# Performance work log

Hardware: AMD Instinct MI355X
Metric: run time of the kernel (lower is better)

The kernel has to match this reference:

```python
import jax, jax.numpy as jnp
import numpy as np

EMBED_DIM = 1024
NUM_HEADS = 16
HEAD_DIM = EMBED_DIM // NUM_HEADS

def setup_inputs() -> dict:
    key = jax.random.key(0)
    k1, k2, k3 = jax.random.split(key, 3)
    x = jax.random.normal(k1, (4, 2048, EMBED_DIM), dtype=jnp.float32)
    # Linear weights stored as [out, in] like torch; we apply x @ W.T
    W_qkv = jax.random.normal(k2, (3 * EMBED_DIM, EMBED_DIM), dtype=jnp.float32) * (EMBED_DIM ** -0.5)
    W_proj = jax.random.normal(k3, (EMBED_DIM, EMBED_DIM), dtype=jnp.float32) * (EMBED_DIM ** -0.5)
    return {"x": x, "W_qkv": W_qkv, "W_proj": W_proj}

def reference(x, W_qkv, W_proj):
    B, T, C = x.shape
    H, D = NUM_HEADS, HEAD_DIM
    qkv = x @ W_qkv.T                          # [B,T,3C]
    q, k, v = jnp.split(qkv, 3, axis=-1)
    q = q.reshape(B, T, H, D).transpose(0, 2, 1, 3)  # [B,H,T,D]
    k = k.reshape(B, T, H, D).transpose(0, 2, 1, 3)
    v = v.reshape(B, T, H, D).transpose(0, 2, 1, 3)
    scores = jnp.einsum('bhqd,bhkd->bhqk', q, k) / jnp.sqrt(jnp.asarray(D, x.dtype))
    causal = jnp.tril(jnp.ones((T, T), dtype=bool))
    scores = jnp.where(causal, scores, -jnp.inf)
    weights = jax.nn.softmax(scores, axis=-1)
    out = jnp.einsum('bhqk,bhkd->bhqd', weights, v)  # [B,H,T,D]
    out = out.transpose(0, 2, 1, 3).reshape(B, T, C)
    return out @ W_proj.T
```

## Files before the change

kernel.cpp:

```cpp
#include <hip/hip_runtime.h>

#define T_SEQ 2048
#define NB 4
#define NH 16
#define HD 64
#define CDIM 1024
#define MROWS (NB * T_SEQ)

typedef __attribute__((ext_vector_type(8))) short short8;
typedef __attribute__((ext_vector_type(4))) float floatx4;

static __device__ __forceinline__ unsigned short f2bf(float f) {
  union { float f; unsigned int i; } c; c.f = f;
  return (unsigned short)((c.i + 0x7FFFu + ((c.i >> 16) & 1u)) >> 16);
}
static __device__ __forceinline__ unsigned short f2bf_trunc(float f) {
  union { float f; unsigned int i; } c; c.f = f;
  return (unsigned short)(c.i >> 16);
}

static __device__ __forceinline__ void gl2lds16(const void* g, void* l) {
  __builtin_amdgcn_global_load_lds(
      (const __attribute__((address_space(1))) unsigned int*)g,
      (__attribute__((address_space(3))) unsigned int*)l, 16, 0, 0);
}

#define X4 (MROWS * CDIM / 4)
#define WQ4 (3 * CDIM * CDIM / 4)
#define WP4 (CDIM * CDIM / 4)
__global__ __launch_bounds__(256) void cast3_bf16(const float* __restrict__ x,
                                                  const float* __restrict__ wq,
                                                  const float* __restrict__ wp,
                                                  unsigned short* __restrict__ out) {
  const int i = blockIdx.x * 256 + threadIdx.x;
  const float* src; int off;
  if (i < X4) { src = x; off = i; }
  else if (i < X4 + WQ4) { src = wq; off = i - X4; }
  else { src = wp; off = i - X4 - WQ4; }
  const float4 v = ((const float4*)src)[off];
  ushort4 o;
  o.x = f2bf(v.x); o.y = f2bf(v.y); o.z = f2bf(v.z); o.w = f2bf(v.w);
  ((ushort4*)out)[i] = o;
}

#define Q_PRESCALE 0.18033688f

#define QNT (CDIM / 64)

__global__ __launch_bounds__(512, 2) void gemm_bf16_qkv256(
    const unsigned short* __restrict__ A,
    const unsigned short* __restrict__ B,
    unsigned short* __restrict__ Oq,
    unsigned short* __restrict__ Ok,
    unsigned short* __restrict__ Ovt,
    const int K)
{
  __shared__ __align__(16) unsigned short As[2][2][128 * 64];
  __shared__ __align__(16) unsigned short Bs[2][2][128 * 64];
  const int tid = threadIdx.x;
  const int w = tid >> 6, l = tid & 63;
  const int quad = l >> 4, l15 = l & 15;
  const int wr = w >> 2, wc = w & 3;
  const int m0 = blockIdx.y * 256, n0 = blockIdx.x * 256;

  const int lrow = l >> 3;
  const int lch = ((l & 7) ^ lrow) * 8;
  const unsigned short* Ag = A + (size_t)(m0 + w * 16 + lrow) * K + lch;
  const unsigned short* Bg = B + (size_t)(n0 + w * 16 + lrow) * K + lch;
  const int ld0 = w * 1024, ld1 = w * 1024 + 512;
  const size_t rsk = (size_t)8 * K;

#define STAGE_A(buf, h, kof) do { \
    gl2lds16(Ag + (size_t)(h) * 128 * K + (kof), &As[buf][h][ld0]); \
    gl2lds16(Ag + (size_t)(h) * 128 * K + rsk + (kof), &As[buf][h][ld1]); } while (0)
#define STAGE_B(buf, h, kof) do { \
    gl2lds16(Bg + (size_t)(h) * 128 * K + (kof), &Bs[buf][h][ld0]); \
    gl2lds16(Bg + (size_t)(h) * 128 * K + rsk + (kof), &Bs[buf][h][ld1]); } while (0)

  const int sw7 = l15 & 7;
  const int co0 = (quad ^ sw7) * 8;
  const int co1 = co0 ^ 32;
  const int fb = l15 * 64;
  const unsigned short* Aw0 = &As[0][wr][0];
  const unsigned short* Aw1 = &As[1][wr][0];
  const unsigned short* Bw0 = &Bs[0][wc >> 1][(wc & 1) * 4096];
  const unsigned short* Bw1 = &Bs[1][wc >> 1][(wc & 1) * 4096];

  floatx4 acc[8][4];
#pragma unroll
  for (int mi = 0; mi < 8; ++mi)
#pragma unroll
    for (int ni = 0; ni < 4; ++ni) acc[mi][ni] = (floatx4){0.f, 0.f, 0.f, 0.f};

  STAGE_A(0, 0, 0); STAGE_A(0, 1, 0); STAGE_B(0, 0, 0); STAGE_B(0, 1, 0);
  STAGE_B(1, 0, 64); STAGE_A(1, 0, 64);
  asm volatile("s_waitcnt vmcnt(4)" ::: "memory");
  __builtin_amdgcn_s_barrier();

#pragma unroll 1
  for (int j = 0; j < QNT; ++j) {
    const int cur = j & 1, nxt = cur ^ 1;
    const unsigned short* Ac = cur ? Aw1 : Aw0;
    const unsigned short* Bc = cur ? Bw1 : Bw0;
    const int kA = (j + 1) * 64, kC = (j + 2) * 64;
    short8 aF[2][4], bL[2][2], bH[2][2];

#pragma unroll
    for (int mi = 0; mi < 4; ++mi) {
      aF[0][mi] = *(const short8*)(Ac + mi * 1024 + fb + co0);
      aF[1][mi] = *(const short8*)(Ac + mi * 1024 + fb + co1);
    }
#pragma unroll
    for (int ni = 0; ni < 2; ++ni) {
      bL[0][ni] = *(const short8*)(Bc + ni * 1024 + fb + co0);
      bL[1][ni] = *(const short8*)(Bc + ni * 1024 + fb + co1);
    }
    if (j + 1 < QNT) STAGE_A(nxt, 1, kA);
    __builtin_amdgcn_s_barrier();
    asm volatile("s_waitcnt lgkmcnt(0)" ::: "memory");
    __builtin_amdgcn_s_setprio(1);
#pragma unroll
    for (int ks = 0; ks < 2; ++ks)
#pragma unroll
      for (int mi = 0; mi < 4; ++mi)
#pragma unroll
        for (int ni = 0; ni < 2; ++ni)
          acc[mi][ni] = __builtin_amdgcn_mfma_f32_16x16x32_bf16(
              bL[ks][ni], aF[ks][mi], acc[mi][ni], 0, 0, 0);
    __builtin_amdgcn_s_setprio(0);
    __builtin_amdgcn_s_barrier();

#pragma unroll
    for (int ni = 0; ni < 2; ++ni) {
      bH[0][ni] = *(const short8*)(Bc + (ni + 2) * 1024 + fb + co0);
      bH[1][ni] = *(const short8*)(Bc + (ni + 2) * 1024 + fb + co1);
    }
    if (j + 1 < QNT) STAGE_B(nxt, 1, kA);
    __builtin_amdgcn_s_barrier();
    asm volatile("s_waitcnt lgkmcnt(0)" ::: "memory");
    __builtin_amdgcn_s_setprio(1);
#pragma unroll
    for (int ks = 0; ks < 2; ++ks)
#pragma unroll
      for (int mi = 0; mi < 4; ++mi)
#pragma unroll
        for (int ni = 0; ni < 2; ++ni)
          acc[mi][ni + 2] = __builtin_amdgcn_mfma_f32_16x16x32_bf16(
              bH[ks][ni], aF[ks][mi], acc[mi][ni + 2], 0, 0, 0);
    __builtin_amdgcn_s_setprio(0);
    __builtin_amdgcn_s_barrier();

#pragma unroll
    for (int mi = 0; mi < 4; ++mi) {
      aF[0][mi] = *(const short8*)(Ac + (mi + 4) * 1024 + fb + co0);
      aF[1][mi] = *(const short8*)(Ac + (mi + 4) * 1024 + fb + co1);
    }
    if (j + 2 < QNT) STAGE_B(cur, 0, kC);
    __builtin_amdgcn_s_barrier();
    asm volatile("s_waitcnt lgkmcnt(0)" ::: "memory");
    __builtin_amdgcn_s_setprio(1);
#pragma unroll
    for (int ks = 0; ks < 2; ++ks)
#pragma unroll
      for (int mi = 0; mi < 4; ++mi)
#pragma unroll
        for (int ni = 0; ni < 2; ++ni)
          acc[mi + 4][ni] = __builtin_amdgcn_mfma_f32_16x16x32_bf16(
              bL[ks][ni], aF[ks][mi], acc[mi + 4][ni], 0, 0, 0);
    __builtin_amdgcn_s_setprio(0);
    __builtin_amdgcn_s_barrier();

    if (j + 2 < QNT) {
      STAGE_A(cur, 0, kC);
      asm volatile("s_waitcnt vmcnt(4)" ::: "memory");
    } else {
      asm volatile("s_waitcnt vmcnt(0)" ::: "memory");
    }
    __builtin_amdgcn_s_barrier();
    __builtin_amdgcn_s_setprio(1);
#pragma unroll
    for (int ks = 0; ks < 2; ++ks)
#pragma unroll
      for (int mi = 0; mi < 4; ++mi)
#pragma unroll
        for (int ni = 0; ni < 2; ++ni)
          acc[mi + 4][ni + 2] = __builtin_amdgcn_mfma_f32_16x16x32_bf16(
              bH[ks][ni], aF[ks][mi], acc[mi + 4][ni + 2], 0, 0, 0);
    __builtin_amdgcn_s_setprio(0);
    __builtin_amdgcn_s_barrier();
  }
#undef STAGE_A
#undef STAGE_B

  const int which = n0 >> 10;
  if (which < 2) {
    unsigned short* dst = (which == 0) ? Oq : Ok;
    const float sc = (which == 0) ? Q_PRESCALE : 1.0f;
#pragma unroll
    for (int ni = 0; ni < 4; ++ni) {
      const int n = n0 + wc * 64 + ni * 16 + quad * 4;
      const int h = (n >> 6) & (NH - 1), d = n & (HD - 1);
#pragma unroll
      for (int mi = 0; mi < 8; ++mi) {
        const int m = m0 + wr * 128 + mi * 16 + l15;
        const int b = m >> 11, t = m & (T_SEQ - 1);
        ushort4 pk;
        pk.x = f2bf(acc[mi][ni][0] * sc); pk.y = f2bf(acc[mi][ni][1] * sc);
        pk.z = f2bf(acc[mi][ni][2] * sc); pk.w = f2bf(acc[mi][ni][3] * sc);
        *(ushort4*)(dst + (((size_t)(b * NH + h) * T_SEQ + t) << 6) + d) = pk;
      }
    }
  } else {
#pragma unroll
    for (int ni = 0; ni < 4; ++ni) {
      const int nb = n0 + wc * 64 + ni * 16 + quad * 4;
      const int h = (nb >> 6) & (NH - 1);
#pragma unroll
      for (int mi = 0; mi < 8; ++mi) {
        const int m = m0 + wr * 128 + mi * 16 + l15;
        const int b = m >> 11, t = m & (T_SEQ - 1);
#pragma unroll
        for (int r = 0; r < 4; ++r) {
          const int d = (nb + r) & (HD - 1);
          Ovt[((size_t)((b * NH + h) * HD + d) << 11) + t] = f2bf(acc[mi][ni][r]);
        }
      }
    }
  }
}

__global__ __launch_bounds__(256) void gemm_bf16_proj(
    const unsigned short* __restrict__ A,
    const unsigned short* __restrict__ B,
    float* __restrict__ O,
    const int N, const int K)
{
  __shared__ unsigned short As[2][128 * 32];
  __shared__ unsigned short Bs[2][128 * 32];
  const int tid = threadIdx.x;
  const int w = tid >> 6, l = tid & 63;
  const int quad = l >> 4, l15 = l & 15;
  const int m0 = blockIdx.y * 128, n0 = blockIdx.x * 128;
  const int wm = (w >> 1) * 64, wn = (w & 1) * 64;
  const int srow = l >> 2;
  const int scol = ((l & 3) ^ (srow & 3)) * 8;

  floatx4 acc[4][4];
#pragma unroll
  for (int mi = 0; mi < 4; ++mi)
#pragma unroll
    for (int ni = 0; ni < 4; ++ni) acc[mi][ni] = (floatx4){0.f, 0.f, 0.f, 0.f};

  const unsigned short* Ag = A + (size_t)(m0 + w * 32 + srow) * K + scol;
  const unsigned short* Bg = B + (size_t)(n0 + w * 32 + srow) * K + scol;
  const int d0 = (w * 32) * 32, d1 = (w * 32 + 16) * 32;
  const int sq = quad ^ (l15 & 3);

  gl2lds16(Ag, &As[0][d0]);
  gl2lds16(Ag + (size_t)16 * K, &As[0][d1]);
  gl2lds16(Bg, &Bs[0][d0]);
  gl2lds16(Bg + (size_t)16 * K, &Bs[0][d1]);

  for (int k0 = 0; k0 < K; k0 += 32) {
    const int cur = (k0 >> 5) & 1, nxt = 1 - cur;
    __syncthreads();
    if (k0 + 32 < K) {
      gl2lds16(Ag + k0 + 32, &As[nxt][d0]);
      gl2lds16(Ag + (size_t)16 * K + k0 + 32, &As[nxt][d1]);
      gl2lds16(Bg + k0 + 32, &Bs[nxt][d0]);
      gl2lds16(Bg + (size_t)16 * K + k0 + 32, &Bs[nxt][d1]);
    }
    short8 af[4], bfr[4];
#pragma unroll
    for (int mi = 0; mi < 4; ++mi)
      af[mi] = *(const short8*)&As[cur][(wm + mi * 16 + l15) * 32 + sq * 8];
#pragma unroll
    for (int ni = 0; ni < 4; ++ni)
      bfr[ni] = *(const short8*)&Bs[cur][(wn + ni * 16 + l15) * 32 + sq * 8];
#pragma unroll
    for (int mi = 0; mi < 4; ++mi)
#pragma unroll
      for (int ni = 0; ni < 4; ++ni)
        acc[mi][ni] = __builtin_amdgcn_mfma_f32_16x16x32_bf16(bfr[ni], af[mi], acc[mi][ni], 0, 0, 0);
  }

#pragma unroll
  for (int ni = 0; ni < 4; ++ni) {
    const int n = n0 + wn + ni * 16 + quad * 4;
#pragma unroll
    for (int mi = 0; mi < 4; ++mi) {
      const int m = m0 + wm + mi * 16 + l15;
      *(float4*)(O + (size_t)m * N + n) =
          make_float4(acc[mi][ni][0], acc[mi][ni][1], acc[mi][ni][2], acc[mi][ni][3]);
    }
  }
}

#define TK 64
#define PTP 72

__global__ __launch_bounds__(512) void attn_mfma(
    const unsigned short* __restrict__ Q,
    const unsigned short* __restrict__ K,
    const unsigned short* __restrict__ Vt,
    unsigned short* __restrict__ O)
{
  __shared__ unsigned short Ks[2][TK * HD];
  __shared__ unsigned short Vts[2][HD * TK];
  __shared__ unsigned short Pt[8][16 * PTP];
  const int tid = threadIdx.x;
  const int w = tid >> 6, l = tid & 63;
  const int quad = l >> 4, l15 = l & 15;
  const int drow = 8 * w + (l >> 3);
  const int dch = ((l & 7) ^ (l >> 3)) * 8;
  const int sw7 = l15 & 7;

  const int bh = blockIdx.x & 63;
  const int pp = blockIdx.x >> 6;
  const int b = bh >> 4, h = bh & 15;
  const size_t hoff = (size_t)bh * T_SEQ * HD;
  const unsigned short* Qh = Q + hoff;
  const unsigned short* Kdma = K + hoff + (size_t)drow * HD + dch;
  const unsigned short* Vdma = Vt + hoff + ((size_t)drow << 11) + dch;
  const int wb = w * 512;

  short8 ones;
#pragma unroll
  for (int j = 0; j < 8; ++j) ones[j] = (short)0x3F80;

#pragma unroll 1
  for (int ii = 0; ii < 2; ++ii) {
    const int qtile = ii ? pp : (15 - pp);
    const int qw = qtile * 128 + w * 16;

    short8 qf[2];
    {
      const int qrow = qw + l15;
      qf[0] = *(const short8*)(Qh + (size_t)qrow * HD + quad * 8);
      qf[1] = *(const short8*)(Qh + (size_t)qrow * HD + 32 + quad * 8);
    }

    floatx4 Of[4];
#pragma unroll
    for (int dc = 0; dc < 4; ++dc) Of[dc] = (floatx4){0.f, 0.f, 0.f, 0.f};
    floatx4 lacc = (floatx4){0.f, 0.f, 0.f, 0.f};

    const int nkt = 2 * qtile + 2;
    __syncthreads();
    gl2lds16(Kdma, &Ks[0][wb]);
    gl2lds16(Vdma, &Vts[0][wb]);

    for (int kt = 0; kt < nkt; ++kt) {
      const int kt0 = kt * TK;
      const int cur = kt & 1, nxt = 1 - cur;
      __syncthreads();
      if (kt + 1 < nkt) {
        gl2lds16(Kdma + (size_t)(kt0 + TK) * HD, &Ks[nxt][wb]);
        gl2lds16(Vdma + kt0 + TK, &Vts[nxt][wb]);
      }

      if (qw + 15 >= kt0) {
        floatx4 Sf[4];
#pragma unroll
        for (int cb = 0; cb < 4; ++cb) {
          Sf[cb] = (floatx4){0.f, 0.f, 0.f, 0.f};
          const int krow = cb * 16 + l15;
#pragma unroll
          for (int h2 = 0; h2 < 2; ++h2) {
            const int ch = (h2 * 4 + quad) ^ sw7;
            const short8 kf = *(const short8*)&Ks[cur][krow * 64 + ch * 8];
            Sf[cb] = __builtin_amdgcn_mfma_f32_16x16x32_bf16(kf, qf[h2], Sf[cb], 0, 0, 0);
          }
        }
        const bool full = (kt0 + 63 <= qw);
        const int q = qw + l15;
#pragma unroll
        for (int cb = 0; cb < 4; ++cb) {
          const int key0 = kt0 + cb * 16 + quad * 4;
          ushort4 pk;
          if (full) {
            pk.x = f2bf_trunc(exp2f(Sf[cb][0]));
            pk.y = f2bf_trunc(exp2f(Sf[cb][1]));
            pk.z = f2bf_trunc(exp2f(Sf[cb][2]));
            pk.w = f2bf_trunc(exp2f(Sf[cb][3]));
          } else {
            pk.x = (key0 + 0 > q) ? 0 : f2bf_trunc(exp2f(Sf[cb][0]));
            pk.y = (key0 + 1 > q) ? 0 : f2bf_trunc(exp2f(Sf[cb][1]));
            pk.z = (key0 + 2 > q) ? 0 : f2bf_trunc(exp2f(Sf[cb][2]));
            pk.w = (key0 + 3 > q) ? 0 : f2bf_trunc(exp2f(Sf[cb][3]));
          }
          *(ushort4*)&Pt[w][l15 * PTP + cb * 16 + quad * 4] = pk;
        }
#pragma unroll
        for (int kg = 0; kg < 2; ++kg) {
          const short8 ptf = *(const short8*)&Pt[w][l15 * PTP + kg * 32 + quad * 8];
          lacc = __builtin_amdgcn_mfma_f32_16x16x32_bf16(ones, ptf, lacc, 0, 0, 0);
#pragma unroll
          for (int dc = 0; dc < 4; ++dc) {
            const int vrow = dc * 16 + l15;
            const int ch = (kg * 4 + quad) ^ sw7;
            const short8 vf = *(const short8*)&Vts[cur][vrow * 64 + ch * 8];
            Of[dc] = __builtin_amdgcn_mfma_f32_16x16x32_bf16(vf, ptf, Of[dc], 0, 0, 0);
          }
        }
      }
    }

    const float inv = 1.f / lacc[0];
    const int q = qw + l15;
    unsigned short* orow = O + (size_t)(b * T_SEQ + q) * CDIM + h * HD + quad * 4;
#pragma unroll
    for (int dc = 0; dc < 4; ++dc) {
      ushort4 ov;
      ov.x = f2bf(Of[dc][0] * inv); ov.y = f2bf(Of[dc][1] * inv);
      ov.z = f2bf(Of[dc][2] * inv); ov.w = f2bf(Of[dc][3] * inv);
      *(ushort4*)(orow + dc * 16) = ov;
    }
  }
}

extern "C" void kernel_launch(void* const* d_in, const int* in_sizes, int n_in,
                              void* d_out, int out_size, void* d_ws, size_t ws_size,
                              hipStream_t stream) {
  const float* x     = (const float*)d_in[0];
  const float* Wqkv  = (const float*)d_in[1];
  const float* Wproj = (const float*)d_in[2];
  float* out = (float*)d_out;

  const size_t XSZ = (size_t)MROWS * CDIM;
  const size_t WQSZ = (size_t)3 * CDIM * CDIM;
  const size_t WPSZ = (size_t)CDIM * CDIM;
  unsigned short* xb  = (unsigned short*)d_ws;
  unsigned short* wqb = xb + XSZ;
  unsigned short* wpb = wqb + WQSZ;
  unsigned short* qbuf = wpb + WPSZ;
  unsigned short* kbuf = qbuf + XSZ;
  unsigned short* vtbuf = kbuf + XSZ;
  unsigned short* abuf = vtbuf + XSZ;

  cast3_bf16<<<(X4 + WQ4 + WP4) / 256, 256, 0, stream>>>(x, Wqkv, Wproj, xb);

  dim3 g1(3 * CDIM / 256, MROWS / 256);
  gemm_bf16_qkv256<<<g1, 512, 0, stream>>>(xb, wqb, qbuf, kbuf, vtbuf, CDIM);

  attn_mfma<<<512, 512, 0, stream>>>(qbuf, kbuf, vtbuf, abuf);

  dim3 g3(CDIM / 128, MROWS / 128);
  gemm_bf16_proj<<<g3, 256, 0, stream>>>(abuf, wpb, out, CDIM, CDIM);
}
```

Baseline: 254.2 us.

## Rewrite projection GEMM as 256x128 pipelined kernel and swizzle QKV block order

The output projection GEMM moves from a 128x128 tile with 256 threads and K-step 32 to a 256x128 tile with 512 threads. It uses K-step 64, split A staging, explicit waitcnt and barrier scheduling, and setprio around the MFMA bursts, following the structure of the QKV kernel. The aim is more data reuse per block and better overlap of global-to-LDS loads with MFMA work. Separately, the QKV GEMM remaps block indices so that concurrently running blocks (likely one group per XCD) share A and B tiles in cache. The costs are higher register and LDS pressure, and a grid of only 256 blocks for the projection.

```diff
diff --git a/kernel.cpp b/kernel.cpp
--- a/kernel.cpp
+++ b/kernel.cpp
@@ -61,7 +61,9 @@
   const int w = tid >> 6, l = tid & 63;
   const int quad = l >> 4, l15 = l & 15;
   const int wr = w >> 2, wc = w & 3;
-  const int m0 = blockIdx.y * 256, n0 = blockIdx.x * 256;
+  const int lin = blockIdx.y * 12 + blockIdx.x;
+  const int swz = (lin & 7) * 48 + (lin >> 3);
+  const int m0 = (swz / 12) * 256, n0 = (swz % 12) * 256;
 
   const int lrow = l >> 3;
   const int lch = ((l & 7) ^ lrow) * 8;
@@ -229,68 +231,119 @@
   }
 }
 
-__global__ __launch_bounds__(256) void gemm_bf16_proj(
+__global__ __launch_bounds__(512, 2) void gemm_bf16_proj256(
     const unsigned short* __restrict__ A,
     const unsigned short* __restrict__ B,
     float* __restrict__ O,
-    const int N, const int K)
+    const int K)
 {
-  __shared__ unsigned short As[2][128 * 32];
-  __shared__ unsigned short Bs[2][128 * 32];
+  __shared__ __align__(16) unsigned short As[2][2][128 * 64];
+  __shared__ __align__(16) unsigned short Bs2[2][128 * 64];
   const int tid = threadIdx.x;
   const int w = tid >> 6, l = tid & 63;
   const int quad = l >> 4, l15 = l & 15;
-  const int m0 = blockIdx.y * 128, n0 = blockIdx.x * 128;
-  const int wm = (w >> 1) * 64, wn = (w & 1) * 64;
-  const int srow = l >> 2;
-  const int scol = ((l & 3) ^ (srow & 3)) * 8;
-
-  floatx4 acc[4][4];
-#pragma unroll
-  for (int mi = 0; mi < 4; ++mi)
-#pragma unroll
-    for (int ni = 0; ni < 4; ++ni) acc[mi][ni] = (floatx4){0.f, 0.f, 0.f, 0.f};
-
-  const unsigned short* Ag = A + (size_t)(m0 + w * 32 + srow) * K + scol;
-  const unsigned short* Bg = B + (size_t)(n0 + w * 32 + srow) * K + scol;
-  const int d0 = (w * 32) * 32, d1 = (w * 32 + 16) * 32;
-  const int sq = quad ^ (l15 & 3);
-
-  gl2lds16(Ag, &As[0][d0]);
-  gl2lds16(Ag + (size_t)16 * K, &As[0][d1]);
-  gl2lds16(Bg, &Bs[0][d0]);
-  gl2lds16(Bg + (size_t)16 * K, &Bs[0][d1]);
-
-  for (int k0 = 0; k0 < K; k0 += 32) {
-    const int cur = (k0 >> 5) & 1, nxt = 1 - cur;
-    __syncthreads();
-    if (k0 + 32 < K) {
-      gl2lds16(Ag + k0 + 32, &As[nxt][d0]);
-      gl2lds16(Ag + (size_t)16 * K + k0 + 32, &As[nxt][d1]);
-      gl2lds16(Bg + k0 + 32, &Bs[nxt][d0]);
-      gl2lds16(Bg + (size_t)16 * K + k0 + 32, &Bs[nxt][d1]);
-    }
-    short8 af[4], bfr[4];
-#pragma unroll
-    for (int mi = 0; mi < 4; ++mi)
-      af[mi] = *(const short8*)&As[cur][(wm + mi * 16 + l15) * 32 + sq * 8];
-#pragma unroll
-    for (int ni = 0; ni < 4; ++ni)
-      bfr[ni] = *(const short8*)&Bs[cur][(wn + ni * 16 + l15) * 32 + sq * 8];
-#pragma unroll
-    for (int mi = 0; mi < 4; ++mi)
-#pragma unroll
-      for (int ni = 0; ni < 4; ++ni)
-        acc[mi][ni] = __builtin_amdgcn_mfma_f32_16x16x32_bf16(bfr[ni], af[mi], acc[mi][ni], 0, 0, 0);
+  const int wr = w >> 2, wc = w & 3;
+  const int m0 = blockIdx.y * 256, n0 = blockIdx.x * 128;
+
+  const int lrow = l >> 3;
+  const int lch = ((l & 7) ^ lrow) * 8;
+  const unsigned short* Ag = A + (size_t)(m0 + w * 16 + lrow) * K + lch;
+  const unsigned short* Bg = B + (size_t)(n0 + w * 16 + lrow) * K + lch;
+  const int ld0 = w * 1024, ld1 = w * 1024 + 512;
+  const size_t rsk = (size_t)8 * K;
+
+#define STAGE_A(buf, h, kof) do { \
+    gl2lds16(Ag + (size_t)(h) * 128 * K + (kof), &As[buf][h][ld0]); \
+    gl2lds16(Ag + (size_t)(h) * 128 * K + rsk + (kof), &As[buf][h][ld1]); } while (0)
+#define STAGE_B(buf, kof) do { \
+    gl2lds16(Bg + (kof), &Bs2[buf][ld0]); \
+    gl2lds16(Bg + rsk + (kof), &Bs2[buf][ld1]); } while (0)
+
+  const int sw7 = l15 & 7;
+  const int co0 = (quad ^ sw7) * 8;
+  const int co1 = co0 ^ 32;
+  const int fb = l15 * 64;
+  const unsigned short* Aw0 = &As[0][wr][0];
+  const unsigned short* Aw1 = &As[1][wr][0];
+  const unsigned short* Bw0 = &Bs2[0][wc * 2048];
+  const unsigned short* Bw1 = &Bs2[1][wc * 2048];
+
+  floatx4 acc[8][2];
+#pragma unroll
+  for (int mi = 0; mi < 8; ++mi)
+#pragma unroll
+    for (int ni = 0; ni < 2; ++ni) acc[mi][ni] = (floatx4){0.f, 0.f, 0.f, 0.f};
+
+  STAGE_A(0, 0, 0); STAGE_A(0, 1, 0); STAGE_B(0, 0);
+  STAGE_A(1, 0, 64);
+  asm volatile("s_waitcnt vmcnt(2)" ::: "memory");
+  __builtin_amdgcn_s_barrier();
+
+#pragma unroll 1
+  for (int j = 0; j < QNT; ++j) {
+    const int cur = j & 1, nxt = cur ^ 1;
+    const unsigned short* Ac = cur ? Aw1 : Aw0;
+    const unsigned short* Bc = cur ? Bw1 : Bw0;
+    const int kA = (j + 1) * 64, kB = (j + 2) * 64;
+    short8 aF[2][4], bF[2][2];
+
+#pragma unroll
+    for (int mi = 0; mi < 4; ++mi) {
+      aF[0][mi] = *(const short8*)(Ac + mi * 1024 + fb + co0);
+      aF[1][mi] = *(const short8*)(Ac + mi * 1024 + fb + co1);
+    }
+#pragma unroll
+    for (int ni = 0; ni < 2; ++ni) {
+      bF[0][ni] = *(const short8*)(Bc + ni * 1024 + fb + co0);
+      bF[1][ni] = *(const short8*)(Bc + ni * 1024 + fb + co1);
+    }
+    if (j + 1 < QNT) { STAGE_A(nxt, 1, kA); STAGE_B(nxt, kA); }
+    __builtin_amdgcn_s_barrier();
+    asm volatile("s_waitcnt lgkmcnt(0)" ::: "memory");
+    __builtin_amdgcn_s_setprio(1);
+#pragma unroll
+    for (int ks = 0; ks < 2; ++ks)
+#pragma unroll
+      for (int mi = 0; mi < 4; ++mi)
+#pragma unroll
+        for (int ni = 0; ni < 2; ++ni)
+          acc[mi][ni] = __builtin_amdgcn_mfma_f32_16x16x32_bf16(
+              bF[ks][ni], aF[ks][mi], acc[mi][ni], 0, 0, 0);
+    __builtin_amdgcn_s_setprio(0);
+    __builtin_amdgcn_s_barrier();
+
+#pragma unroll
+    for (int mi = 0; mi < 4; ++mi) {
+      aF[0][mi] = *(const short8*)(Ac + (mi + 4) * 1024 + fb + co0);
+      aF[1][mi] = *(const short8*)(Ac + (mi + 4) * 1024 + fb + co1);
+    }
+    if (j + 2 < QNT) STAGE_A(cur, 0, kB);
+    __builtin_amdgcn_s_barrier();
+    asm volatile("s_waitcnt lgkmcnt(0)" ::: "memory");
+    __builtin_amdgcn_s_setprio(1);
+#pragma unroll
+    for (int ks = 0; ks < 2; ++ks)
+#pragma unroll
+      for (int mi = 0; mi < 4; ++mi)
+#pragma unroll
+        for (int ni = 0; ni < 2; ++ni)
+          acc[mi + 4][ni] = __builtin_amdgcn_mfma_f32_16x16x32_bf16(
+              bF[ks][ni], aF[ks][mi], acc[mi + 4][ni], 0, 0, 0);
+    __builtin_amdgcn_s_setprio(0);
+    if (j + 2 < QNT) asm volatile("s_waitcnt vmcnt(2)" ::: "memory");
+    else             asm volatile("s_waitcnt vmcnt(0)" ::: "memory");
+    __builtin_amdgcn_s_barrier();
   }
-
-#pragma unroll
-  for (int ni = 0; ni < 4; ++ni) {
-    const int n = n0 + wn + ni * 16 + quad * 4;
-#pragma unroll
-    for (int mi = 0; mi < 4; ++mi) {
-      const int m = m0 + wm + mi * 16 + l15;
-      *(float4*)(O + (size_t)m * N + n) =
+#undef STAGE_A
+#undef STAGE_B
+
+#pragma unroll
+  for (int ni = 0; ni < 2; ++ni) {
+    const int n = n0 + wc * 32 + ni * 16 + quad * 4;
+#pragma unroll
+    for (int mi = 0; mi < 8; ++mi) {
+      const int m = m0 + wr * 128 + mi * 16 + l15;
+      *(float4*)(O + (size_t)m * CDIM + n) =
           make_float4(acc[mi][ni][0], acc[mi][ni][1], acc[mi][ni][2], acc[mi][ni][3]);
     }
   }
@@ -445,6 +498,6 @@
 
   attn_mfma<<<512, 512, 0, stream>>>(qbuf, kbuf, vtbuf, abuf);
 
-  dim3 g3(CDIM / 128, MROWS / 128);
-  gemm_bf16_proj<<<g3, 256, 0, stream>>>(abuf, wpb, out, CDIM, CDIM);
-}
+  dim3 g3(CDIM / 128, MROWS / 256);
+  gemm_bf16_proj256<<<g3, 512, 0, stream>>>(abuf, wpb, out, CDIM);
+}
```

After: 252.6 us. About the same (-0.6%).
